# Kernel tuning notes

Hardware: AMD Instinct MI355X
Metric: run time of the kernel (lower is better)

## Reference

```python
import jax, jax.numpy as jnp
import numpy as np

METRIC = (1.0, 1.0, 1.0, 1.0, -1.0)  # Cl(4,1) signature
N_HEADS = 8
EPS = 1e-6


def _cayley():
    # Cayley table C[a, b, k]: e_a * e_b = sum_k C[a,b,k] e_k, blades indexed by bitmask over 5 generators.
    C = np.zeros((32, 32, 32), dtype=np.float32)
    for a in range(32):
        for b in range(32):
            s = 0
            t = a >> 1
            while t:
                s += bin(t & b).count('1')
                t >>= 1
            sign = -1.0 if (s & 1) else 1.0
            for i in range(5):
                if (a & b) >> i & 1:
                    sign *= METRIC[i]
            C[a, b, a ^ b] = sign
    return C

_C_NP = _cayley()
GP_MAP = jnp.asarray(_C_NP)  # (32,32,32)
SIG = jnp.asarray(_C_NP[np.arange(32), np.arange(32), 0])  # blade square signs, (32,)


def normalize_cl41(x):
    # normalize each multivector (last-dim 32 blades) to unit RMS
    return x / jnp.sqrt(jnp.mean(x * x, axis=-1, keepdims=True) + EPS)


def versor_linear(x, W):
    # x: (B,S,I,32), W: (O,I,32); out_k = sum_{i,j,l} W[o,i,j] C[j,l,k] x[b,s,i,l]
    O, I, _ = W.shape
    W_op = jnp.einsum('oij,jlk->oilk', W, GP_MAP)  # (O,I,32,32)
    W_mat = W_op.transpose(1, 2, 0, 3).reshape(I * 32, O * 32)
    B, S = x.shape[0], x.shape[1]
    out = (x.reshape(B, S, I * 32) @ W_mat).reshape(B, S, O, 32)
    return normalize_cl41(out)


def versor_attention(x, Wq, Wk, Wv, Wo, lam):
    B, S, D, _ = x.shape
    H = N_HEADS
    hd = D // H

    def split_heads(t):  # (B,S,D,32) -> (B,H,S,hd,32)
        return t.reshape(B, S, H, hd, 32).transpose(0, 2, 1, 3, 4)

    q = split_heads(versor_linear(x, Wq))
    k = split_heads(versor_linear(x, Wk))
    v = split_heads(versor_linear(x, Wv))

    q_flat = (q * SIG).reshape(B, H, S, hd * 32)  # signature-weighted
    k_flat = k.reshape(B, H, S, hd * 32)

    scalar = jnp.einsum('bhsd,bhtd->bhst', q_flat, k_flat)
    scale = 1.0 / jnp.sqrt(jnp.asarray(hd, x.dtype))
    score = scalar * scale

    # torque term: sqrt(relu(|q|^2 |k|^2 - (q.k)^2) + eps) / sqrt(hd)
    q_norm_sq = jnp.sum(q_flat * q_flat, axis=-1)[..., :, None]  # (B,H,S,1)
    k_norm_sq = jnp.sum(k_flat * k_flat, axis=-1)[..., None, :]  # (B,H,1,S)
    torque = jnp.sqrt(jax.nn.relu(q_norm_sq * k_norm_sq - scalar * scalar) + EPS) * scale
    score = score + lam * torque

    probs = jax.nn.softmax(score, axis=-1)
    out = jnp.einsum('bhst,bhtdl->bhsdl', probs, v)  # (B,H,S,hd,32)
    out = out.transpose(0, 2, 1, 3, 4).reshape(B, S, D, 32)
    return versor_linear(out, Wo)


def setup_inputs() -> dict:
    key = jax.random.key(0)
    ks = jax.random.split(key, 5)
    B, S, D = 2, 1024, 128
    std = (2.0 / (D * 32)) ** 0.5  # Versor init
    x = jax.random.normal(ks[0], (B, S, D, 32), jnp.float32)
    Wq = jax.random.normal(ks[1], (D, D, 32), jnp.float32) * std
    Wk = jax.random.normal(ks[2], (D, D, 32), jnp.float32) * std
    Wv = jax.random.normal(ks[3], (D, D, 32), jnp.float32) * std
    Wo = jax.random.normal(ks[4], (D, D, 32), jnp.float32) * std
    attn_lambda = jnp.float32(0.1)
    return {'x': x, 'Wq': Wq, 'Wk': Wk, 'Wv': Wv, 'Wo': Wo, 'attn_lambda': attn_lambda}


def reference(x, Wq, Wk, Wv, Wo, attn_lambda):
    return versor_attention(x, Wq, Wk, Wv, Wo, attn_lambda)
```

## Files before the change

### kernel.cpp

```cpp
#include <hip/hip_runtime.h>
#include <stdint.h>

typedef __attribute__((ext_vector_type(4))) float    f32x4;
typedef __attribute__((ext_vector_type(8))) short    s16x8;
typedef __attribute__((ext_vector_type(4))) short    s16x4;
typedef __attribute__((ext_vector_type(8))) _Float16 f16x8;

#define DEV __device__ __forceinline__

DEV float blade_sign(int a, int b){
    int s = 0, t = a >> 1;
    while (t){ s += __popc(t & b); t >>= 1; }
    float sg = (s & 1) ? -1.0f : 1.0f;
    return ((a & b) & 16) ? -sg : sg;
}
DEV short f2h(float v){
    _Float16 h = (_Float16)v;
    return __builtin_bit_cast(short, h);
}
DEV float h2f(short b){
    return (float)__builtin_bit_cast(_Float16, b);
}

__global__ __launch_bounds__(256) void cast_f32_f16(const float* __restrict__ in,
                                                    short* __restrict__ out){
    const size_t idx = (size_t)blockIdx.x * 256 + threadIdx.x;
    const float4* p = reinterpret_cast<const float4*>(in) + idx * 2;
    float4 a = p[0], b = p[1];
    s16x8 o;
    o[0]=f2h(a.x); o[1]=f2h(a.y); o[2]=f2h(a.z); o[3]=f2h(a.w);
    o[4]=f2h(b.x); o[5]=f2h(b.y); o[6]=f2h(b.z); o[7]=f2h(b.w);
    *reinterpret_cast<s16x8*>(out + idx * 8) = o;
}

DEV void build_wmat_body(const float* __restrict__ W, short* __restrict__ WmT,
                         int idx){
    const int n  = idx >> 9;
    const int kg = idx & 511;
    const int o = n >> 5, kb = n & 31;
    const int i = kg >> 2, l0 = (kg & 3) * 8;
    const float* wrow = W + (size_t)(o * 128 + i) * 32;
    s16x8 v;
    #pragma unroll
    for (int e = 0; e < 8; ++e){
        const int l = l0 + e, j = kb ^ l;
        v[e] = f2h(wrow[j] * blade_sign(j, l));
    }
    *reinterpret_cast<s16x8*>(WmT + (size_t)n * 4096 + kg * 8) = v;
}

__global__ __launch_bounds__(256) void build_wmat(const float* __restrict__ W,
                                                  short* __restrict__ WmT){
    build_wmat_body(W, WmT, blockIdx.x * 256 + threadIdx.x);
}

__global__ __launch_bounds__(256) void build_wmat3(const float* __restrict__ Wq,
                                                   const float* __restrict__ Wk,
                                                   const float* __restrict__ Wv,
                                                   short* __restrict__ WmT3){
    const int w = blockIdx.y;
    const float* W = (w == 0) ? Wq : ((w == 1) ? Wk : Wv);
    build_wmat_body(W, WmT3 + (size_t)w * 4096 * 4096,
                    blockIdx.x * 256 + threadIdx.x);
}

__global__ __launch_bounds__(256) void row_norms(const short* __restrict__ Q,
                                                 const short* __restrict__ Kq,
                                                 float* __restrict__ Nq,
                                                 float* __restrict__ Nk){
    const int row  = blockIdx.x * 4 + (threadIdx.x >> 6);
    const int lane = threadIdx.x & 63;
    const int b = row >> 13, h = (row >> 10) & 7, s = row & 1023;
    const size_t off = ((size_t)(b * 1024 + s)) * 4096 + h * 512 + lane * 8;
    s16x8 a = *reinterpret_cast<const s16x8*>(Q + off);
    s16x8 c = *reinterpret_cast<const s16x8*>(Kq + off);
    float sq = 0.f, sk = 0.f;
    #pragma unroll
    for (int e = 0; e < 8; ++e){
        float fa = h2f(a[e]); sq = fmaf(fa, fa, sq);
        float fc = h2f(c[e]); sk = fmaf(fc, fc, sk);
    }
    #pragma unroll
    for (int m = 1; m < 64; m <<= 1){
        sq += __shfl_xor(sq, m);
        sk += __shfl_xor(sk, m);
    }
    if (lane == 0){ Nq[row] = sq; Nk[row] = sk; }
}

__global__ __launch_bounds__(256) void softmax_rows(float* __restrict__ Sc){
    const int row  = blockIdx.x * 4 + (threadIdx.x >> 6);
    const int lane = threadIdx.x & 63;
    float* p = Sc + (size_t)row * 1024;
    float v[16];
    float mx = -3.0e38f;
    #pragma unroll
    for (int j = 0; j < 16; ++j){ v[j] = p[lane + j * 64]; mx = fmaxf(mx, v[j]); }
    #pragma unroll
    for (int m = 1; m < 64; m <<= 1) mx = fmaxf(mx, __shfl_xor(mx, m));
    float sum = 0.f;
    #pragma unroll
    for (int j = 0; j < 16; ++j){ v[j] = __expf(v[j] - mx); sum += v[j]; }
    #pragma unroll
    for (int m = 1; m < 64; m <<= 1) sum += __shfl_xor(sum, m);
    const float inv = 1.0f / sum;
    short* pb = reinterpret_cast<short*>(p);
    #pragma unroll
    for (int j = 0; j < 16; ++j) pb[lane + j * 64] = f2h(v[j] * inv);
}

#define GLOAD_LDS(gp, lp) \
    __builtin_amdgcn_global_load_lds( \
        (const __attribute__((address_space(1))) void*)(const void*)(gp), \
        (__attribute__((address_space(3))) void*)(void*)(lp), 16, 0, 0)

template<int EPI>
__global__ __launch_bounds__(512, 2) void versor_gemm8(
    const short* __restrict__ Abase, int lda,
    const short* __restrict__ Bbase, int ldb,
    int K, void* __restrict__ OutP,
    const float* __restrict__ NqP, const float* __restrict__ NkP,
    const float* __restrict__ LamP,
    short* __restrict__ OQ, short* __restrict__ OK, short* __restrict__ OV)
{
    extern __shared__ short lds[];

    const int tid  = threadIdx.x;
    const int lane = tid & 63;
    const int wid  = tid >> 6;
    const int wm   = wid >> 2;
    const int wn   = wid & 3;
    const int z    = blockIdx.z;

    const short* A = Abase;
    const short* B = Bbase;
    if constexpr (EPI == 4){
        const int b = z >> 3, h = z & 7;
        const size_t off = (size_t)b * 1024 * 4096 + (size_t)h * 512;
        A += off; B += off;
    }
    const int row0 = blockIdx.y * 256;
    const int col0 = blockIdx.x * 256;

    const int jsw = ((lane & 3) ^ ((lane >> 3) & 3)) * 8;
    const short* gA0 = A + (size_t)(row0 + wid * 32 + (lane >> 2)) * lda + jsw;
    const short* gA1 = gA0 + (size_t)16 * lda;
    const short* gB0 = B + (size_t)(col0 + wid * 32 + (lane >> 2)) * ldb + jsw;
    const short* gB1 = gB0 + (size_t)16 * ldb;
    const int dA0 = wid * 1024, dA1 = dA0 + 512;
    const int dB0 = 8192 + wid * 1024, dB1 = dB0 + 512;

    const int swz = ((lane >> 4) ^ (((lane & 15) >> 1) & 3)) * 8;
    const int ard = (wm * 128 + (lane & 15)) * 32 + swz;
    const int brd = 8192 + (wn * 64 + (lane & 15)) * 32 + swz;

    f32x4 acc[8][4];
    #pragma unroll
    for (int i = 0; i < 8; ++i)
        #pragma unroll
        for (int j = 0; j < 4; ++j)
            acc[i][j] = (f32x4){0.f, 0.f, 0.f, 0.f};

    const int NT = K >> 5;

    #pragma unroll
    for (int pt = 0; pt < 3; ++pt){
        const int bb = pt * 16384;
        GLOAD_LDS(gA0 + pt * 32, lds + bb + dA0);
        GLOAD_LDS(gA1 + pt * 32, lds + bb + dA1);
        GLOAD_LDS(gB0 + pt * 32, lds + bb + dB0);
        GLOAD_LDS(gB1 + pt * 32, lds + bb + dB1);
    }

    for (int t = 0; t < NT; ++t){
        const int bb = (t & 3) * 16384;
        asm volatile("s_waitcnt vmcnt(8)" ::: "memory");
        __builtin_amdgcn_s_barrier();
        asm volatile("" ::: "memory");
        __builtin_amdgcn_sched_barrier(0);

        if (t + 3 < NT){
            const int nb = ((t + 3) & 3) * 16384;
            GLOAD_LDS(gA0 + (t + 3) * 32, lds + nb + dA0);
            GLOAD_LDS(gA1 + (t + 3) * 32, lds + nb + dA1);
        }
        f16x8 av[4], bv[4];
        #pragma unroll
        for (int i = 0; i < 4; ++i){
            av[i] = *reinterpret_cast<const f16x8*>(lds + bb + ard + i * 512);
            bv[i] = *reinterpret_cast<const f16x8*>(lds + bb + brd + i * 512);
        }
        __builtin_amdgcn_s_setprio(1);
        #pragma unroll
        for (int mi = 0; mi < 4; ++mi)
            #pragma unroll
            for (int ni = 0; ni < 4; ++ni)
                acc[mi][ni] = __builtin_amdgcn_mfma_f32_16x16x32_f16(
                    av[mi], bv[ni], acc[mi][ni], 0, 0, 0);
        __builtin_amdgcn_s_setprio(0);

        if (t + 3 < NT){
            const int nb = ((t + 3) & 3) * 16384;
            GLOAD_LDS(gB0 + (t + 3) * 32, lds + nb + dB0);
            GLOAD_LDS(gB1 + (t + 3) * 32, lds + nb + dB1);
        }
        f16x8 aw[4];
        #pragma unroll
        for (int i = 0; i < 4; ++i)
            aw[i] = *reinterpret_cast<const f16x8*>(lds + bb + ard + (4 + i) * 512);
        __builtin_amdgcn_s_setprio(1);
        #pragma unroll
        for (int mi = 0; mi < 4; ++mi)
            #pragma unroll
            for (int ni = 0; ni < 4; ++ni)
                acc[4 + mi][ni] = __builtin_amdgcn_mfma_f32_16x16x32_f16(
                    aw[mi], bv[ni], acc[4 + mi][ni], 0, 0, 0);
        __builtin_amdgcn_s_setprio(0);
    }

    const int rb = row0 + wm * 128 + (lane >> 4) * 4;
    const int cb = col0 + wn * 64 + (lane & 15);

    if constexpr (EPI == 0 || EPI == 3){
        #pragma unroll
        for (int mi = 0; mi < 8; ++mi){
            #pragma unroll
            for (int g = 0; g < 2; ++g){
                f32x4 a0 = acc[mi][2 * g], a1 = acc[mi][2 * g + 1];
                f32x4 ss = a0 * a0 + a1 * a1;
                #pragma unroll
                for (int m = 1; m < 16; m <<= 1){
                    ss.x += __shfl_xor(ss.x, m);
                    ss.y += __shfl_xor(ss.y, m);
                    ss.z += __shfl_xor(ss.z, m);
                    ss.w += __shfl_xor(ss.w, m);
                }
                f32x4 inv;
                inv.x = 1.0f / sqrtf(ss.x * 0.03125f + 1e-6f);
                inv.y = 1.0f / sqrtf(ss.y * 0.03125f + 1e-6f);
                inv.z = 1.0f / sqrtf(ss.z * 0.03125f + 1e-6f);
                inv.w = 1.0f / sqrtf(ss.w * 0.03125f + 1e-6f);
                acc[mi][2 * g]     = a0 * inv;
                acc[mi][2 * g + 1] = a1 * inv;
            }
        }
    }

    if constexpr (EPI == 0){
        const int zsel = col0 >> 12;
        const int cbm  = (col0 & 4095) + wn * 64 + (lane & 15);
        if (zsel == 0){
            const float sg0 = blade_sign(lane & 15, lane & 15);
            const float sg1 = blade_sign(16 | (lane & 15), 16 | (lane & 15));
            #pragma unroll
            for (int mi = 0; mi < 8; ++mi)
                #pragma unroll
                for (int ni = 0; ni < 4; ++ni){
                    const f32x4 v = acc[mi][ni] * ((ni & 1) ? sg1 : sg0);
                    #pragma unroll
                    for (int j = 0; j < 4; ++j)
                        OQ[(size_t)(rb + mi * 16 + j) * 4096 + (cbm + ni * 16)] = f2h(v[j]);
                }
        } else if (zsel == 1){
            #pragma unroll
            for (int mi = 0; mi < 8; ++mi)
                #pragma unroll
                for (int ni = 0; ni < 4; ++ni)
                    #pragma unroll
                    for (int j = 0; j < 4; ++j)
                        OK[(size_t)(rb + mi * 16 + j) * 4096 + (cbm + ni * 16)] = f2h(acc[mi][ni][j]);
        } else {
            #pragma unroll
            for (int mi = 0; mi < 8; ++mi){
                const int r = rb + mi * 16;
                const int b = r >> 10, tt = r & 1023;
                #pragma unroll
                for (int ni = 0; ni < 4; ++ni){
                    const int c = cbm + ni * 16;
                    const int h = c >> 9, f = c & 511;
                    s16x4 pv;
                    #pragma unroll
                    for (int j = 0; j < 4; ++j) pv[j] = f2h(acc[mi][ni][j]);
                    *reinterpret_cast<s16x4*>(OV + ((size_t)((b * 8 + h) * 512 + f)) * 1024 + tt) = pv;
                }
            }
        }
    }
    if constexpr (EPI == 3){
        float* Of = (float*)OutP;
        #pragma unroll
        for (int mi = 0; mi < 8; ++mi)
            #pragma unroll
            for (int ni = 0; ni < 4; ++ni)
                #pragma unroll
                for (int j = 0; j < 4; ++j)
                    Of[(size_t)(rb + mi * 16 + j) * 4096 + (cb + ni * 16)] = acc[mi][ni][j];
    }
    if constexpr (EPI == 4){
        float* Of = (float*)OutP + (size_t)z * 1024 * 1024;
        const float lam = *LamP;
        const float* nq = NqP + z * 1024;
        const float* nk = NkP + z * 1024;
        #pragma unroll
        for (int mi = 0; mi < 8; ++mi)
            #pragma unroll
            for (int j = 0; j < 4; ++j){
                const int r = rb + mi * 16 + j;
                const float qn = nq[r];
                #pragma unroll
                for (int ni = 0; ni < 4; ++ni){
                    const int c = cb + ni * 16;
                    const float sc = acc[mi][ni][j];
                    const float tq = sqrtf(fmaxf(qn * nk[c] - sc * sc, 0.0f) + 1e-6f);
                    Of[(size_t)r * 1024 + c] = 0.25f * (sc + lam * tq);
                }
            }
    }
}

__global__ __launch_bounds__(256) void versor_gemm_pv(
    const short* __restrict__ Abase, int lda,
    const short* __restrict__ Bbase, int ldb,
    int K, short* __restrict__ OutP)
{
    __shared__ short As[128 * 32];
    __shared__ short Bs[128 * 32];

    const int tid  = threadIdx.x;
    const int lane = tid & 63;
    const int wid  = tid >> 6;
    const int wr   = wid >> 1;
    const int wc   = wid & 1;
    const int z    = blockIdx.z;

    const short* A = Abase + (size_t)z * 1024 * 2048;
    const short* B = Bbase + (size_t)z * 512 * 1024;

    const int row0 = blockIdx.y * 128;
    const int col0 = blockIdx.x * 128;

    const int slot0 = (wid * 2 + 0) * 64 + lane;
    const int slot1 = (wid * 2 + 1) * 64 + lane;
    const int ar0 = slot0 >> 2, ac0 = (slot0 & 3) * 8;
    const int ar1 = slot1 >> 2, ac1 = (slot1 & 3) * 8;
    const short* gA0 = A + (size_t)(row0 + ar0) * lda + ac0;
    const short* gA1 = A + (size_t)(row0 + ar1) * lda + ac1;
    const short* gB0 = B + (size_t)(col0 + ar0) * ldb + ac0;
    const short* gB1 = B + (size_t)(col0 + ar1) * ldb + ac1;
    short* lA0 = As + (wid * 2 + 0) * 512;
    short* lA1 = As + (wid * 2 + 1) * 512;
    short* lB0 = Bs + (wid * 2 + 0) * 512;
    short* lB1 = Bs + (wid * 2 + 1) * 512;

    f32x4 acc[4][4];
    #pragma unroll
    for (int i = 0; i < 4; ++i)
        #pragma unroll
        for (int j = 0; j < 4; ++j)
            acc[i][j] = (f32x4){0.f, 0.f, 0.f, 0.f};

    const int fragoff = (lane & 15) * 32 + (lane >> 4) * 8;

    for (int kt = 0; kt < K; kt += 32){
        __syncthreads();
        GLOAD_LDS(gA0 + kt, lA0);
        GLOAD_LDS(gA1 + kt, lA1);
        GLOAD_LDS(gB0 + kt, lB0);
        GLOAD_LDS(gB1 + kt, lB1);
        __syncthreads();

        f16x8 af[4], bfv[4];
        #pragma unroll
        for (int i = 0; i < 4; ++i){
            af[i]  = *reinterpret_cast<const f16x8*>(As + (wr * 64 + i * 16) * 32 + fragoff);
            bfv[i] = *reinterpret_cast<const f16x8*>(Bs + (wc * 64 + i * 16) * 32 + fragoff);
        }
        #pragma unroll
        for (int mi = 0; mi < 4; ++mi)
            #pragma unroll
            for (int ni = 0; ni < 4; ++ni)
                acc[mi][ni] = __builtin_amdgcn_mfma_f32_16x16x32_f16(
                    af[mi], bfv[ni], acc[mi][ni], 0, 0, 0);
    }

    const int rb = row0 + wr * 64 + (lane >> 4) * 4;
    const int cb = col0 + wc * 64 + (lane & 15);
    const int b = z >> 3, h = z & 7;
    #pragma unroll
    for (int mi = 0; mi < 4; ++mi)
        #pragma unroll
        for (int ni = 0; ni < 4; ++ni)
            #pragma unroll
            for (int j = 0; j < 4; ++j)
                OutP[(size_t)(b * 1024 + rb + mi * 16 + j) * 4096 + h * 512 + (cb + ni * 16)]
                    = f2h(acc[mi][ni][j]);
}

extern "C" void kernel_launch(void* const* d_in, const int* in_sizes, int n_in,
                              void* d_out, int out_size, void* d_ws, size_t ws_size,
                              hipStream_t stream)
{
    (void)in_sizes; (void)n_in; (void)out_size; (void)ws_size;
    const float* x   = (const float*)d_in[0];
    const float* Wq  = (const float*)d_in[1];
    const float* Wk  = (const float*)d_in[2];
    const float* Wv  = (const float*)d_in[3];
    const float* Wo  = (const float*)d_in[4];
    const float* lam = (const float*)d_in[5];
    float* out = (float*)d_out;
    char*  ws  = (char*)d_ws;

    short* Xf   = (short*)(ws);
    short* WmT3 = (short*)(ws + (16u  << 20));
    short* Qf   = (short*)(ws + (112u << 20));
    short* Kf   = (short*)(ws + (128u << 20));
    short* Vt   = (short*)(ws + (144u << 20));
    float* Nq   = (float*)(ws + (160u << 20));
    float* Nk   = (float*)(ws + (160u << 20) + (64u << 10));
    float* Sc   = (float*)(ws + (16u  << 20));
    short* WmTo = (short*)(ws + (80u  << 20));
    short* Attn = Xf;

    const int DYN_LDS = 131072;
    hipFuncSetAttribute(reinterpret_cast<const void*>(versor_gemm8<0>),
                        hipFuncAttributeMaxDynamicSharedMemorySize, DYN_LDS);
    hipFuncSetAttribute(reinterpret_cast<const void*>(versor_gemm8<3>),
                        hipFuncAttributeMaxDynamicSharedMemorySize, DYN_LDS);
    hipFuncSetAttribute(reinterpret_cast<const void*>(versor_gemm8<4>),
                        hipFuncAttributeMaxDynamicSharedMemorySize, DYN_LDS);

    dim3 blk(256), blk8(512);
    cast_f32_f16<<<4096, blk, 0, stream>>>(x, Xf);

    dim3 gw3(8192, 3);
    build_wmat3<<<gw3, blk, 0, stream>>>(Wq, Wk, Wv, WmT3);

    dim3 gqkv(48, 8, 1);
    versor_gemm8<0><<<gqkv, blk8, DYN_LDS, stream>>>(
        Xf, 4096, WmT3, 4096, 4096, nullptr, nullptr, nullptr, nullptr, Qf, Kf, Vt);

    row_norms<<<4096, blk, 0, stream>>>(Qf, Kf, Nq, Nk);

    build_wmat<<<8192, blk, 0, stream>>>(Wo, WmTo);

    dim3 gsc(4, 4, 16);
    versor_gemm8<4><<<gsc, blk8, DYN_LDS, stream>>>(
        Qf, 4096, Kf, 4096, 512, Sc, Nq, Nk, lam, nullptr, nullptr, nullptr);
    softmax_rows<<<4096, blk, 0, stream>>>(Sc);

    dim3 gpv(4, 8, 16);
    versor_gemm_pv<<<gpv, blk, 0, stream>>>((const short*)Sc, 2048, Vt, 1024, 1024, Attn);

    dim3 gfin(16, 8, 1);
    versor_gemm8<3><<<gfin, blk8, DYN_LDS, stream>>>(
        Attn, 4096, WmTo, 4096, 4096, out, nullptr, nullptr, nullptr, nullptr, nullptr, nullptr);
}
```

Measured before the change: 571.9 us.

## Switch QKV, PV and output GEMMs to 128x128 tiles with triple-buffered pipeline

Replaces the 256x256, 512-thread GEMM with a 128x128, 256-thread kernel using 3 static LDS stages and 3 blocks per CU for QKV projection, PV and output projection. The PV GEMM, previously a synchronous single-buffer kernel, now uses the pipelined one. The score GEMM is split into its own kernel with a peeled tail so the final vmcnt waits drain correctly. This aims for more blocks and better CU occupancy and latency hiding, at the cost of less operand reuse per tile.

```diff
diff --git a/kernel.cpp b/kernel.cpp
--- a/kernel.cpp
+++ b/kernel.cpp
@@ -20,6 +20,11 @@
 }
 DEV float h2f(short b){
     return (float)__builtin_bit_cast(_Float16, b);
+}
+DEV void wait_vm(int n){
+    if (n == 8)      asm volatile("s_waitcnt vmcnt(8)" ::: "memory");
+    else if (n == 4) asm volatile("s_waitcnt vmcnt(4)" ::: "memory");
+    else             asm volatile("s_waitcnt vmcnt(0)" ::: "memory");
 }
 
 __global__ __launch_bounds__(256) void cast_f32_f16(const float* __restrict__ in,
@@ -114,49 +119,90 @@
         (const __attribute__((address_space(1))) void*)(const void*)(gp), \
         (__attribute__((address_space(3))) void*)(void*)(lp), 16, 0, 0)
 
+#define R3_TILE(T, WN, PF)                                                      \
+  {                                                                             \
+    const int bb = cur * 8192;                                                  \
+    wait_vm(WN);                                                                \
+    __builtin_amdgcn_s_barrier();                                               \
+    asm volatile("" ::: "memory");                                              \
+    __builtin_amdgcn_sched_barrier(0);                                          \
+    const int sb = stg * 8192;                                                  \
+    if (PF){                                                                    \
+        GLOAD_LDS(gA0 + (size_t)((T) + 2) * 32, lds + sb + dA0);                \
+        GLOAD_LDS(gA1 + (size_t)((T) + 2) * 32, lds + sb + dA1);                \
+    }                                                                           \
+    f16x8 av[4], bv[4];                                                         \
+    _Pragma("unroll")                                                           \
+    for (int i = 0; i < 4; ++i)                                                 \
+        av[i] = *reinterpret_cast<const f16x8*>(lds + bb + ard + i * 512);      \
+    bv[0] = *reinterpret_cast<const f16x8*>(lds + bb + brd + 0 * 512);          \
+    bv[1] = *reinterpret_cast<const f16x8*>(lds + bb + brd + 1 * 512);          \
+    __builtin_amdgcn_s_setprio(1);                                              \
+    _Pragma("unroll")                                                           \
+    for (int mi = 0; mi < 4; ++mi)                                              \
+        _Pragma("unroll")                                                       \
+        for (int ni = 0; ni < 2; ++ni)                                          \
+            acc[mi][ni] = __builtin_amdgcn_mfma_f32_16x16x32_f16(               \
+                av[mi], bv[ni], acc[mi][ni], 0, 0, 0);                          \
+    __builtin_amdgcn_s_setprio(0);                                              \
+    if (PF){                                                                    \
+        GLOAD_LDS(gB0 + (size_t)((T) + 2) * 32, lds + sb + dB0);                \
+        GLOAD_LDS(gB1 + (size_t)((T) + 2) * 32, lds + sb + dB1);                \
+    }                                                                           \
+    bv[2] = *reinterpret_cast<const f16x8*>(lds + bb + brd + 2 * 512);          \
+    bv[3] = *reinterpret_cast<const f16x8*>(lds + bb + brd + 3 * 512);          \
+    __builtin_amdgcn_s_setprio(1);                                              \
+    _Pragma("unroll")                                                           \
+    for (int mi = 0; mi < 4; ++mi)                                              \
+        _Pragma("unroll")                                                       \
+        for (int ni = 2; ni < 4; ++ni)                                          \
+            acc[mi][ni] = __builtin_amdgcn_mfma_f32_16x16x32_f16(               \
+                av[mi], bv[ni], acc[mi][ni], 0, 0, 0);                          \
+    __builtin_amdgcn_s_setprio(0);                                              \
+    cur = (cur == 2) ? 0 : cur + 1;                                             \
+    stg = (stg == 2) ? 0 : stg + 1;                                             \
+  }
+
 template<int EPI>
-__global__ __launch_bounds__(512, 2) void versor_gemm8(
+__global__ __launch_bounds__(256, 3) void versor_gemm_r3(
     const short* __restrict__ Abase, int lda,
     const short* __restrict__ Bbase, int ldb,
     int K, void* __restrict__ OutP,
-    const float* __restrict__ NqP, const float* __restrict__ NkP,
-    const float* __restrict__ LamP,
     short* __restrict__ OQ, short* __restrict__ OK, short* __restrict__ OV)
 {
-    extern __shared__ short lds[];
+    __shared__ short lds[3 * 8192];
 
     const int tid  = threadIdx.x;
     const int lane = tid & 63;
     const int wid  = tid >> 6;
-    const int wm   = wid >> 2;
-    const int wn   = wid & 3;
+    const int wr   = wid >> 1;
+    const int wc   = wid & 1;
     const int z    = blockIdx.z;
 
     const short* A = Abase;
     const short* B = Bbase;
-    if constexpr (EPI == 4){
-        const int b = z >> 3, h = z & 7;
-        const size_t off = (size_t)b * 1024 * 4096 + (size_t)h * 512;
-        A += off; B += off;
-    }
-    const int row0 = blockIdx.y * 256;
-    const int col0 = blockIdx.x * 256;
+    if constexpr (EPI == 5){
+        A += (size_t)z * 1024 * 2048;
+        B += (size_t)z * 512 * 1024;
+    }
+    const int row0 = blockIdx.y * 128;
+    const int col0 = blockIdx.x * 128;
 
     const int jsw = ((lane & 3) ^ ((lane >> 3) & 3)) * 8;
-    const short* gA0 = A + (size_t)(row0 + wid * 32 + (lane >> 2)) * lda + jsw;
-    const short* gA1 = gA0 + (size_t)16 * lda;
-    const short* gB0 = B + (size_t)(col0 + wid * 32 + (lane >> 2)) * ldb + jsw;
-    const short* gB1 = gB0 + (size_t)16 * ldb;
-    const int dA0 = wid * 1024, dA1 = dA0 + 512;
-    const int dB0 = 8192 + wid * 1024, dB1 = dB0 + 512;
+    const short* gA0 = A + (size_t)(row0 + wid * 16 + (lane >> 2)) * lda + jsw;
+    const short* gA1 = gA0 + (size_t)64 * lda;
+    const short* gB0 = B + (size_t)(col0 + wid * 16 + (lane >> 2)) * ldb + jsw;
+    const short* gB1 = gB0 + (size_t)64 * ldb;
+    const int dA0 = wid * 512,        dA1 = 2048 + wid * 512;
+    const int dB0 = 4096 + wid * 512, dB1 = 6144 + wid * 512;
 
     const int swz = ((lane >> 4) ^ (((lane & 15) >> 1) & 3)) * 8;
-    const int ard = (wm * 128 + (lane & 15)) * 32 + swz;
-    const int brd = 8192 + (wn * 64 + (lane & 15)) * 32 + swz;
-
-    f32x4 acc[8][4];
-    #pragma unroll
-    for (int i = 0; i < 8; ++i)
+    const int ard = (wr * 64 + (lane & 15)) * 32 + swz;
+    const int brd = 4096 + (wc * 64 + (lane & 15)) * 32 + swz;
+
+    f32x4 acc[4][4];
+    #pragma unroll
+    for (int i = 0; i < 4; ++i)
         #pragma unroll
         for (int j = 0; j < 4; ++j)
             acc[i][j] = (f32x4){0.f, 0.f, 0.f, 0.f};
@@ -164,66 +210,25 @@
     const int NT = K >> 5;
 
     #pragma unroll
-    for (int pt = 0; pt < 3; ++pt){
-        const int bb = pt * 16384;
-        GLOAD_LDS(gA0 + pt * 32, lds + bb + dA0);
-        GLOAD_LDS(gA1 + pt * 32, lds + bb + dA1);
-        GLOAD_LDS(gB0 + pt * 32, lds + bb + dB0);
-        GLOAD_LDS(gB1 + pt * 32, lds + bb + dB1);
-    }
-
-    for (int t = 0; t < NT; ++t){
-        const int bb = (t & 3) * 16384;
-        asm volatile("s_waitcnt vmcnt(8)" ::: "memory");
-        __builtin_amdgcn_s_barrier();
-        asm volatile("" ::: "memory");
-        __builtin_amdgcn_sched_barrier(0);
-
-        if (t + 3 < NT){
-            const int nb = ((t + 3) & 3) * 16384;
-            GLOAD_LDS(gA0 + (t + 3) * 32, lds + nb + dA0);
-            GLOAD_LDS(gA1 + (t + 3) * 32, lds + nb + dA1);
-        }
-        f16x8 av[4], bv[4];
-        #pragma unroll
-        for (int i = 0; i < 4; ++i){
-            av[i] = *reinterpret_cast<const f16x8*>(lds + bb + ard + i * 512);
-            bv[i] = *reinterpret_cast<const f16x8*>(lds + bb + brd + i * 512);
-        }
-        __builtin_amdgcn_s_setprio(1);
-        #pragma unroll
-        for (int mi = 0; mi < 4; ++mi)
-            #pragma unroll
-            for (int ni = 0; ni < 4; ++ni)
-                acc[mi][ni] = __builtin_amdgcn_mfma_f32_16x16x32_f16(
-                    av[mi], bv[ni], acc[mi][ni], 0, 0, 0);
-        __builtin_amdgcn_s_setprio(0);
-
-        if (t + 3 < NT){
-            const int nb = ((t + 3) & 3) * 16384;
-            GLOAD_LDS(gB0 + (t + 3) * 32, lds + nb + dB0);
-            GLOAD_LDS(gB1 + (t + 3) * 32, lds + nb + dB1);
-        }
-        f16x8 aw[4];
-        #pragma unroll
-        for (int i = 0; i < 4; ++i)
-            aw[i] = *reinterpret_cast<const f16x8*>(lds + bb + ard + (4 + i) * 512);
-        __builtin_amdgcn_s_setprio(1);
-        #pragma unroll
-        for (int mi = 0; mi < 4; ++mi)
-            #pragma unroll
-            for (int ni = 0; ni < 4; ++ni)
-                acc[4 + mi][ni] = __builtin_amdgcn_mfma_f32_16x16x32_f16(
-                    aw[mi], bv[ni], acc[4 + mi][ni], 0, 0, 0);
-        __builtin_amdgcn_s_setprio(0);
-    }
-
-    const int rb = row0 + wm * 128 + (lane >> 4) * 4;
-    const int cb = col0 + wn * 64 + (lane & 15);
+    for (int pt = 0; pt < 2; ++pt){
+        const int sb = pt * 8192;
+        GLOAD_LDS(gA0 + pt * 32, lds + sb + dA0);
+        GLOAD_LDS(gA1 + pt * 32, lds + sb + dA1);
+        GLOAD_LDS(gB0 + pt * 32, lds + sb + dB0);
+        GLOAD_LDS(gB1 + pt * 32, lds + sb + dB1);
+    }
+
+    int cur = 0, stg = 2;
+    for (int t = 0; t < NT - 1; ++t)
+        R3_TILE(t, 4, (t + 2 < NT))
+    R3_TILE(NT - 1, 0, false)
+
+    const int rb = row0 + wr * 64 + (lane >> 4) * 4;
+    const int cb = col0 + wc * 64 + (lane & 15);
 
     if constexpr (EPI == 0 || EPI == 3){
         #pragma unroll
-        for (int mi = 0; mi < 8; ++mi){
+        for (int mi = 0; mi < 4; ++mi){
             #pragma unroll
             for (int g = 0; g < 2; ++g){
                 f32x4 a0 = acc[mi][2 * g], a1 = acc[mi][2 * g + 1];
@@ -248,12 +253,12 @@
 
     if constexpr (EPI == 0){
         const int zsel = col0 >> 12;
-        const int cbm  = (col0 & 4095) + wn * 64 + (lane & 15);
+        const int cbm  = (col0 & 4095) + wc * 64 + (lane & 15);
         if (zsel == 0){
             const float sg0 = blade_sign(lane & 15, lane & 15);
             const float sg1 = blade_sign(16 | (lane & 15), 16 | (lane & 15));
             #pragma unroll
-            for (int mi = 0; mi < 8; ++mi)
+            for (int mi = 0; mi < 4; ++mi)
                 #pragma unroll
                 for (int ni = 0; ni < 4; ++ni){
                     const f32x4 v = acc[mi][ni] * ((ni & 1) ? sg1 : sg0);
@@ -263,7 +268,7 @@
                 }
         } else if (zsel == 1){
             #pragma unroll
-            for (int mi = 0; mi < 8; ++mi)
+            for (int mi = 0; mi < 4; ++mi)
                 #pragma unroll
                 for (int ni = 0; ni < 4; ++ni)
                     #pragma unroll
@@ -271,7 +276,7 @@
                         OK[(size_t)(rb + mi * 16 + j) * 4096 + (cbm + ni * 16)] = f2h(acc[mi][ni][j]);
         } else {
             #pragma unroll
-            for (int mi = 0; mi < 8; ++mi){
+            for (int mi = 0; mi < 4; ++mi){
                 const int r = rb + mi * 16;
                 const int b = r >> 10, tt = r & 1023;
                 #pragma unroll
@@ -289,111 +294,151 @@
     if constexpr (EPI == 3){
         float* Of = (float*)OutP;
         #pragma unroll
-        for (int mi = 0; mi < 8; ++mi)
+        for (int mi = 0; mi < 4; ++mi)
             #pragma unroll
             for (int ni = 0; ni < 4; ++ni)
                 #pragma unroll
                 for (int j = 0; j < 4; ++j)
                     Of[(size_t)(rb + mi * 16 + j) * 4096 + (cb + ni * 16)] = acc[mi][ni][j];
     }
-    if constexpr (EPI == 4){
-        float* Of = (float*)OutP + (size_t)z * 1024 * 1024;
-        const float lam = *LamP;
-        const float* nq = NqP + z * 1024;
-        const float* nk = NkP + z * 1024;
-        #pragma unroll
-        for (int mi = 0; mi < 8; ++mi)
-            #pragma unroll
-            for (int j = 0; j < 4; ++j){
-                const int r = rb + mi * 16 + j;
-                const float qn = nq[r];
-                #pragma unroll
-                for (int ni = 0; ni < 4; ++ni){
-                    const int c = cb + ni * 16;
-                    const float sc = acc[mi][ni][j];
-                    const float tq = sqrtf(fmaxf(qn * nk[c] - sc * sc, 0.0f) + 1e-6f);
-                    Of[(size_t)r * 1024 + c] = 0.25f * (sc + lam * tq);
-                }
-            }
-    }
-}
-
-__global__ __launch_bounds__(256) void versor_gemm_pv(
-    const short* __restrict__ Abase, int lda,
-    const short* __restrict__ Bbase, int ldb,
-    int K, short* __restrict__ OutP)
+    if constexpr (EPI == 5){
+        short* Ob = (short*)OutP;
+        const int b = z >> 3, h = z & 7;
+        #pragma unroll
+        for (int mi = 0; mi < 4; ++mi)
+            #pragma unroll
+            for (int ni = 0; ni < 4; ++ni)
+                #pragma unroll
+                for (int j = 0; j < 4; ++j)
+                    Ob[(size_t)(b * 1024 + rb + mi * 16 + j) * 4096 + h * 512 + (cb + ni * 16)]
+                        = f2h(acc[mi][ni][j]);
+    }
+}
+
+#define SC_TILE(T, WN, PF)                                                      \
+  {                                                                             \
+    const int bb = ((T) & 3) * 16384;                                           \
+    wait_vm(WN);                                                                \
+    __builtin_amdgcn_s_barrier();                                               \
+    asm volatile("" ::: "memory");                                              \
+    __builtin_amdgcn_sched_barrier(0);                                          \
+    if (PF){                                                                    \
+        const int nb = (((T) + 3) & 3) * 16384;                                 \
+        GLOAD_LDS(gA0 + (size_t)((T) + 3) * 32, lds + nb + dA0);                \
+        GLOAD_LDS(gA1 + (size_t)((T) + 3) * 32, lds + nb + dA1);                \
+    }                                                                           \
+    f16x8 av[4], bv[4];                                                         \
+    _Pragma("unroll")                                                           \
+    for (int i = 0; i < 4; ++i){                                                \
+        av[i] = *reinterpret_cast<const f16x8*>(lds + bb + ard + i * 512);      \
+        bv[i] = *reinterpret_cast<const f16x8*>(lds + bb + brd + i * 512);      \
+    }                                                                           \
+    __builtin_amdgcn_s_setprio(1);                                              \
+    _Pragma("unroll")                                                           \
+    for (int mi = 0; mi < 4; ++mi)                                              \
+        _Pragma("unroll")                                                       \
+        for (int ni = 0; ni < 4; ++ni)                                          \
+            acc[mi][ni] = __builtin_amdgcn_mfma_f32_16x16x32_f16(               \
+                av[mi], bv[ni], acc[mi][ni], 0, 0, 0);                          \
+    __builtin_amdgcn_s_setprio(0);                                              \
+    if (PF){                                                                    \
+        const int nb = (((T) + 3) & 3) * 16384;                                 \
+        GLOAD_LDS(gB0 + (size_t)((T) + 3) * 32, lds + nb + dB0);                \
+        GLOAD_LDS(gB1 + (size_t)((T) + 3) * 32, lds + nb + dB1);                \
+    }                                                                           \
+    f16x8 aw[4];                                                                \
+    _Pragma("unroll")                                                           \
+    for (int i = 0; i < 4; ++i)                                                 \
+        aw[i] = *reinterpret_cast<const f16x8*>(lds + bb + ard + (4 + i) * 512);\
+    __builtin_amdgcn_s_setprio(1);                                              \
+    _Pragma("unroll")                                                           \
+    for (int mi = 0; mi < 4; ++mi)                                              \
+        _Pragma("unroll")                                                       \
+        for (int ni = 0; ni < 4; ++ni)                                          \
+            acc[4 + mi][ni] = __builtin_amdgcn_mfma_f32_16x16x32_f16(           \
+                aw[mi], bv[ni], acc[4 + mi][ni], 0, 0, 0);                      \
+    __builtin_amdgcn_s_setprio(0);                                              \
+  }
+
+__global__ __launch_bounds__(512, 2) void versor_gemm_sc(
+    const short* __restrict__ Qbase, const short* __restrict__ Kbase,
+    int K, float* __restrict__ OutP,
+    const float* __restrict__ NqP, const float* __restrict__ NkP,
+    const float* __restrict__ LamP)
 {
-    __shared__ short As[128 * 32];
-    __shared__ short Bs[128 * 32];
+    extern __shared__ short lds[];
 
     const int tid  = threadIdx.x;
     const int lane = tid & 63;
     const int wid  = tid >> 6;
-    const int wr   = wid >> 1;
-    const int wc   = wid & 1;
+    const int wm   = wid >> 2;
+    const int wn   = wid & 3;
     const int z    = blockIdx.z;
 
-    const short* A = Abase + (size_t)z * 1024 * 2048;
-    const short* B = Bbase + (size_t)z * 512 * 1024;
-
-    const int row0 = blockIdx.y * 128;
-    const int col0 = blockIdx.x * 128;
-
-    const int slot0 = (wid * 2 + 0) * 64 + lane;
-    const int slot1 = (wid * 2 + 1) * 64 + lane;
-    const int ar0 = slot0 >> 2, ac0 = (slot0 & 3) * 8;
-    const int ar1 = slot1 >> 2, ac1 = (slot1 & 3) * 8;
-    const short* gA0 = A + (size_t)(row0 + ar0) * lda + ac0;
-    const short* gA1 = A + (size_t)(row0 + ar1) * lda + ac1;
-    const short* gB0 = B + (size_t)(col0 + ar0) * ldb + ac0;
-    const short* gB1 = B + (size_t)(col0 + ar1) * ldb + ac1;
-    short* lA0 = As + (wid * 2 + 0) * 512;
-    short* lA1 = As + (wid * 2 + 1) * 512;
-    short* lB0 = Bs + (wid * 2 + 0) * 512;
-    short* lB1 = Bs + (wid * 2 + 1) * 512;
-
-    f32x4 acc[4][4];
-    #pragma unroll
-    for (int i = 0; i < 4; ++i)
+    const int b = z >> 3, h = z & 7;
+    const size_t off = (size_t)b * 1024 * 4096 + (size_t)h * 512;
+    const short* A = Qbase + off;
+    const short* B = Kbase + off;
+    const int lda = 4096, ldb = 4096;
+    const int row0 = blockIdx.y * 256;
+    const int col0 = blockIdx.x * 256;
+
+    const int jsw = ((lane & 3) ^ ((lane >> 3) & 3)) * 8;
+    const short* gA0 = A + (size_t)(row0 + wid * 32 + (lane >> 2)) * lda + jsw;
+    const short* gA1 = gA0 + (size_t)16 * lda;
+    const short* gB0 = B + (size_t)(col0 + wid * 32 + (lane >> 2)) * ldb + jsw;
+    const short* gB1 = gB0 + (size_t)16 * ldb;
+    const int dA0 = wid * 1024, dA1 = dA0 + 512;
+    const int dB0 = 8192 + wid * 1024, dB1 = dB0 + 512;
+
+    const int swz = ((lane >> 4) ^ (((lane & 15) >> 1) & 3)) * 8;
+    const int ard = (wm * 128 + (lane & 15)) * 32 + swz;
+    const int brd = 8192 + (wn * 64 + (lane & 15)) * 32 + swz;
+
+    f32x4 acc[8][4];
+    #pragma unroll
+    for (int i = 0; i < 8; ++i)
         #pragma unroll
         for (int j = 0; j < 4; ++j)
             acc[i][j] = (f32x4){0.f, 0.f, 0.f, 0.f};
 
-    const int fragoff = (lane & 15) * 32 + (lane >> 4) * 8;
-
-    for (int kt = 0; kt < K; kt += 32){
-        __syncthreads();
-        GLOAD_LDS(gA0 + kt, lA0);
-        GLOAD_LDS(gA1 + kt, lA1);
-        GLOAD_LDS(gB0 + kt, lB0);
-        GLOAD_LDS(gB1 + kt, lB1);
-        __syncthreads();
-
-        f16x8 af[4], bfv[4];
-        #pragma unroll
-        for (int i = 0; i < 4; ++i){
-            af[i]  = *reinterpret_cast<const f16x8*>(As + (wr * 64 + i * 16) * 32 + fragoff);
-            bfv[i] = *reinterpret_cast<const f16x8*>(Bs + (wc * 64 + i * 16) * 32 + fragoff);
+    const int NT = K >> 5;
+
+    #pragma unroll
+    for (int pt = 0; pt < 3; ++pt){
+        const int bb = pt * 16384;
+        GLOAD_LDS(gA0 + pt * 32, lds + bb + dA0);
+        GLOAD_LDS(gA1 + pt * 32, lds + bb + dA1);
+        GLOAD_LDS(gB0 + pt * 32, lds + bb + dB0);
+        GLOAD_LDS(gB1 + pt * 32, lds + bb + dB1);
+    }
+
+    for (int t = 0; t < NT - 2; ++t)
+        SC_TILE(t, 8, (t + 3 < NT))
+    SC_TILE(NT - 2, 4, false)
+    SC_TILE(NT - 1, 0, false)
+
+    const int rb = row0 + wm * 128 + (lane >> 4) * 4;
+    const int cb = col0 + wn * 64 + (lane & 15);
+
+    float* Of = OutP + (size_t)z * 1024 * 1024;
+    const float lam = *LamP;
+    const float* nq = NqP + z * 1024;
+    const float* nk = NkP + z * 1024;
+    #pragma unroll
+    for (int mi = 0; mi < 8; ++mi)
+        #pragma unroll
+        for (int j = 0; j < 4; ++j){
+            const int r = rb + mi * 16 + j;
+            const float qn = nq[r];
+            #pragma unroll
+            for (int ni = 0; ni < 4; ++ni){
+                const int c = cb + ni * 16;
+                const float sc = acc[mi][ni][j];
+                const float tq = sqrtf(fmaxf(qn * nk[c] - sc * sc, 0.0f) + 1e-6f);
+                Of[(size_t)r * 1024 + c] = 0.25f * (sc + lam * tq);
+            }
         }
-        #pragma unroll
-        for (int mi = 0; mi < 4; ++mi)
-            #pragma unroll
-            for (int ni = 0; ni < 4; ++ni)
-                acc[mi][ni] = __builtin_amdgcn_mfma_f32_16x16x32_f16(
-                    af[mi], bfv[ni], acc[mi][ni], 0, 0, 0);
-    }
-
-    const int rb = row0 + wr * 64 + (lane >> 4) * 4;
-    const int cb = col0 + wc * 64 + (lane & 15);
-    const int b = z >> 3, h = z & 7;
-    #pragma unroll
-    for (int mi = 0; mi < 4; ++mi)
-        #pragma unroll
-        for (int ni = 0; ni < 4; ++ni)
-            #pragma unroll
-            for (int j = 0; j < 4; ++j)
-                OutP[(size_t)(b * 1024 + rb + mi * 16 + j) * 4096 + h * 512 + (cb + ni * 16)]
-                    = f2h(acc[mi][ni][j]);
 }
 
 extern "C" void kernel_launch(void* const* d_in, const int* in_sizes, int n_in,
@@ -422,11 +467,7 @@
     short* Attn = Xf;
 
     const int DYN_LDS = 131072;
-    hipFuncSetAttribute(reinterpret_cast<const void*>(versor_gemm8<0>),
-                        hipFuncAttributeMaxDynamicSharedMemorySize, DYN_LDS);
-    hipFuncSetAttribute(reinterpret_cast<const void*>(versor_gemm8<3>),
-                        hipFuncAttributeMaxDynamicSharedMemorySize, DYN_LDS);
-    hipFuncSetAttribute(reinterpret_cast<const void*>(versor_gemm8<4>),
+    hipFuncSetAttribute(reinterpret_cast<const void*>(versor_gemm_sc),
                         hipFuncAttributeMaxDynamicSharedMemorySize, DYN_LDS);
 
     dim3 blk(256), blk8(512);
@@ -435,23 +476,23 @@
     dim3 gw3(8192, 3);
     build_wmat3<<<gw3, blk, 0, stream>>>(Wq, Wk, Wv, WmT3);
 
-    dim3 gqkv(48, 8, 1);
-    versor_gemm8<0><<<gqkv, blk8, DYN_LDS, stream>>>(
-        Xf, 4096, WmT3, 4096, 4096, nullptr, nullptr, nullptr, nullptr, Qf, Kf, Vt);
+    dim3 gqkv(96, 16, 1);
+    versor_gemm_r3<0><<<gqkv, blk, 0, stream>>>(
+        Xf, 4096, WmT3, 4096, 4096, nullptr, Qf, Kf, Vt);
 
     row_norms<<<4096, blk, 0, stream>>>(Qf, Kf, Nq, Nk);
 
     build_wmat<<<8192, blk, 0, stream>>>(Wo, WmTo);
 
     dim3 gsc(4, 4, 16);
-    versor_gemm8<4><<<gsc, blk8, DYN_LDS, stream>>>(
-        Qf, 4096, Kf, 4096, 512, Sc, Nq, Nk, lam, nullptr, nullptr, nullptr);
+    versor_gemm_sc<<<gsc, blk8, DYN_LDS, stream>>>(Qf, Kf, 512, Sc, Nq, Nk, lam);
     softmax_rows<<<4096, blk, 0, stream>>>(Sc);
 
     dim3 gpv(4, 8, 16);
-    versor_gemm_pv<<<gpv, blk, 0, stream>>>((const short*)Sc, 2048, Vt, 1024, 1024, Attn);
-
-    dim3 gfin(16, 8, 1);
-    versor_gemm8<3><<<gfin, blk8, DYN_LDS, stream>>>(
-        Attn, 4096, WmTo, 4096, 4096, out, nullptr, nullptr, nullptr, nullptr, nullptr, nullptr);
-}
+    versor_gemm_r3<5><<<gpv, blk, 0, stream>>>(
+        (const short*)Sc, 2048, Vt, 1024, 1024, Attn, nullptr, nullptr, nullptr);
+
+    dim3 gfin(32, 16, 1);
+    versor_gemm_r3<3><<<gfin, blk, 0, stream>>>(
+        Attn, 4096, WmTo, 4096, 4096, out, nullptr, nullptr, nullptr);
+}
```

After: 553.7 us. -3.2%, faster.
